# Kernel optimization log

Measured on AMD Instinct MI355X. Metric: run time of the kernel, lower is better.

## Reference

```python
import jax, jax.numpy as jnp
import numpy as np

INPUT_SIZE = 968
HIDDEN = 128
ESP = 1e-6


def _gru_scan(xp, w_hh, b_hh):
    # xp: [T, B, 3H] precomputed input projections; returns [T, B, H]
    B = xp.shape[1]
    h0 = jnp.zeros((B, HIDDEN), dtype=xp.dtype)

    def step(h, xp_t):
        gi_r, gi_z, gi_n = jnp.split(xp_t, 3, axis=-1)
        gh = h @ w_hh.T + b_hh
        gh_r, gh_z, gh_n = jnp.split(gh, 3, axis=-1)
        r = jax.nn.sigmoid(gi_r + gh_r)
        z = jax.nn.sigmoid(gi_z + gh_z)
        n = jnp.tanh(gi_n + r * gh_n)
        h_new = (1.0 - z) * n + z * h
        return h_new, h_new

    _, hs = jax.lax.scan(step, h0, xp)
    return hs


def _bigru_ln(x, w_ih_f, w_hh_f, b_ih_f, b_hh_f,
              w_ih_b, w_hh_b, b_ih_b, b_hh_b, ln_w, ln_b):
    # x: [B, T, D] (batch_first)
    # precompute input projections as one big GEMM per direction
    xp_f = jnp.einsum('btd,gd->btg', x, w_ih_f) + b_ih_f  # [B,T,3H]
    xp_b = jnp.einsum('btd,gd->btg', x, w_ih_b) + b_ih_b
    xp_f = jnp.swapaxes(xp_f, 0, 1)  # [T,B,3H]
    xp_b = jnp.swapaxes(xp_b, 0, 1)[::-1]  # reversed time for backward dir

    h_f = _gru_scan(xp_f, w_hh_f, b_hh_f)          # [T,B,H]
    h_b = _gru_scan(xp_b, w_hh_b, b_hh_b)[::-1]    # [T,B,H], un-reverse

    out = jnp.concatenate([h_f, h_b], axis=-1)     # [T,B,2H]
    out = jnp.swapaxes(out, 0, 1)                  # [B,T,2H]

    # LayerNormal: uses unbiased std (torch.std default, ddof=1), clamped
    mu = jnp.mean(out, axis=-1, keepdims=True)
    sigma = jnp.std(out, axis=-1, keepdims=True, ddof=1)
    sigma = jnp.maximum(sigma, ESP)
    return (out - mu) / sigma * ln_w + ln_b


def setup_inputs() -> dict:
    key = jax.random.key(0)
    ks = jax.random.split(key, 10)
    B, T = 64, 512
    s_ih = 1.0 / np.sqrt(HIDDEN)
    u = lambda k, shape: jax.random.uniform(k, shape, jnp.float32, -s_ih, s_ih)
    return {
        'x': jax.random.normal(ks[0], (B, T, INPUT_SIZE), jnp.float32),
        'w_ih_f': u(ks[1], (3 * HIDDEN, INPUT_SIZE)),
        'w_hh_f': u(ks[2], (3 * HIDDEN, HIDDEN)),
        'b_ih_f': u(ks[3], (3 * HIDDEN,)),
        'b_hh_f': u(ks[4], (3 * HIDDEN,)),
        'w_ih_b': u(ks[5], (3 * HIDDEN, INPUT_SIZE)),
        'w_hh_b': u(ks[6], (3 * HIDDEN, HIDDEN)),
        'b_ih_b': u(ks[7], (3 * HIDDEN,)),
        'b_hh_b': u(ks[8], (3 * HIDDEN,)),
        'ln_w': jnp.ones((2 * HIDDEN,), jnp.float32),
        'ln_b': jnp.zeros((2 * HIDDEN,), jnp.float32),
    }


def reference(x, w_ih_f, w_hh_f, b_ih_f, b_hh_f,
              w_ih_b, w_hh_b, b_ih_b, b_hh_b, ln_w, ln_b):
    return _bigru_ln(x, w_ih_f, w_hh_f, b_ih_f, b_hh_f,
                     w_ih_b, w_hh_b, b_ih_b, b_hh_b, ln_w, ln_b)
```

## Files before the change

kernel.cpp:

```cpp
#include <hip/hip_runtime.h>
#include <stdint.h>


#define LOG2E 1.4426950408889634f
#define TT 512
#define D_IN 968
#define KP 992
#define NOUT 768
#define HID 128

typedef __attribute__((ext_vector_type(8))) short short8;
typedef __attribute__((ext_vector_type(4))) float f32x4;
typedef __attribute__((ext_vector_type(4))) unsigned int u32x4;
typedef __attribute__((ext_vector_type(2))) unsigned int u32x2;

__device__ __forceinline__ unsigned short f2bf(float f) {
  unsigned u = __builtin_bit_cast(unsigned, f);
  u += 0x7FFFu + ((u >> 16) & 1u);
  return (unsigned short)(u >> 16);
}
__device__ __forceinline__ unsigned pack2bf(float a, float b) {
  return (unsigned)f2bf(a) | ((unsigned)f2bf(b) << 16);
}
__device__ __forceinline__ float exp2_(float x) { return __builtin_amdgcn_exp2f(x); }
__device__ __forceinline__ float rcp_(float x)  { return __builtin_amdgcn_rcpf(x); }

__device__ __forceinline__ void async_load16(const void* g, void* l) {
  __builtin_amdgcn_global_load_lds(
      (const __attribute__((address_space(1))) unsigned int*)g,
      (__attribute__((address_space(3))) unsigned int*)l, 16, 0, 0);
}

__device__ __forceinline__ void wg_barrier_lds() {
  asm volatile("s_waitcnt lgkmcnt(0)\n\ts_barrier" ::: "memory");
}

#define WIH_BYTES (NOUT * KP * 2)
#define WHH_BYTES (NOUT * HID * 2)
#define BIAS_BYTES 3072
#define BASE_OFF (WIH_BYTES + WHH_BYTES + BIAS_BYTES)
#define XBF_BYTES ((size_t)32768 * KP * 2)
#define XP_BYTES ((size_t)32768 * NOUT * 4)

__global__ __launch_bounds__(256) void kx_convert(const float* __restrict__ X,
                                                  unsigned short* __restrict__ Xb) {
  const long row = blockIdx.x;
  const int t = threadIdx.x;
  if (t < 242) {
    f32x4 v = *(const f32x4*)(X + row * D_IN + t * 4);
    u32x2 p = {pack2bf(v.x, v.y), pack2bf(v.z, v.w)};
    *(u32x2*)(Xb + row * KP + t * 4) = p;
  } else if (t < 248) {
    *(u32x2*)(Xb + row * KP + t * 4) = (u32x2){0, 0};
  }
}

__global__ __launch_bounds__(256) void k0_convert(
    const float* __restrict__ wihf, const float* __restrict__ whhf,
    const float* __restrict__ bihf, const float* __restrict__ wihb,
    const float* __restrict__ whhb, const float* __restrict__ bihb,
    unsigned short* __restrict__ wih16, unsigned short* __restrict__ whh16,
    float* __restrict__ bias_s) {
  int blk = blockIdx.x, tid = threadIdx.x;
  if (blk < NOUT) {
    int n = blk;
    float sc = ((n % 384) < 256) ? LOG2E : 2.0f * LOG2E;
    const float* src = (n < 384) ? (wihf + (long)n * D_IN) : (wihb + (long)(n - 384) * D_IN);
    for (int c = 0; c < 4; c++) {
      int k = c * 256 + tid;
      if (k < KP) {
        float v = (k < D_IN) ? src[k] * sc : 0.0f;
        wih16[(long)n * KP + k] = f2bf(v);
      }
    }
  } else if (blk < NOUT + 96) {
    int e0 = ((blk - NOUT) * 256 + tid) * 4;
    for (int i = 0; i < 4; i++) {
      int e = e0 + i;
      int m = e >> 7, k = e & 127;
      float sc = ((m % 384) < 256) ? LOG2E : 2.0f * LOG2E;
      float v = (m < 384) ? whhf[m * HID + k] : whhb[(m - 384) * HID + k];
      whh16[e] = f2bf(v * sc);
    }
  } else {
    for (int c = 0; c < 3; c++) {
      int n = c * 256 + tid;
      if (n < NOUT) {
        float sc = ((n % 384) < 256) ? LOG2E : 2.0f * LOG2E;
        bias_s[n] = ((n < 384) ? bihf[n] : bihb[n - 384]) * sc;
      }
    }
  }
}

__global__ __launch_bounds__(256, 2) void k1_gemm_fast(
    const unsigned short* __restrict__ Xb, const unsigned short* __restrict__ W,
    const float* __restrict__ bias_s, float* __restrict__ XP) {
  __shared__ unsigned short As[128 * 32];
  __shared__ unsigned short Bs[128 * 32];

  const int tid = threadIdx.x;
  const int lane = tid & 63, w = tid >> 6;
  const int q = lane >> 4, l15 = lane & 15;
  const int wr = w >> 1, wc = w & 1;
  const int nt = blockIdx.x;
  const int mt = blockIdx.y;
  const long R0 = (long)mt * 128;
  const int C0 = nt * 128;

  f32x4 acc[4][4];
#pragma unroll
  for (int i = 0; i < 4; i++)
#pragma unroll
    for (int j = 0; j < 4; j++) acc[i][j] = {0.f, 0.f, 0.f, 0.f};

  for (int it = 0; it < 31; it++) {
    const int k0 = it * 32;
#pragma unroll
    for (int c = 0; c < 2; c++) {
      int idx = c * 256 + w * 64 + lane;
      int row = idx >> 2, koff = (idx & 3) * 8;
      async_load16(Xb + (R0 + row) * KP + k0 + koff,
                   ((char*)As) + (c * 256 + w * 64) * 16);
      async_load16(W + (long)(C0 + row) * KP + k0 + koff,
                   ((char*)Bs) + (c * 256 + w * 64) * 16);
    }
    __syncthreads();
    short8 af[4], bf[4];
#pragma unroll
    for (int i = 0; i < 4; i++)
      af[i] = *(const short8*)&As[(wr * 64 + i * 16 + l15) * 32 + q * 8];
#pragma unroll
    for (int j = 0; j < 4; j++)
      bf[j] = *(const short8*)&Bs[(wc * 64 + j * 16 + l15) * 32 + q * 8];
#pragma unroll
    for (int i = 0; i < 4; i++)
#pragma unroll
      for (int j = 0; j < 4; j++)
        acc[i][j] = __builtin_amdgcn_mfma_f32_16x16x32_bf16(af[i], bf[j], acc[i][j], 0, 0, 0);
    __syncthreads();
  }
  float bv[4];
#pragma unroll
  for (int j = 0; j < 4; j++) bv[j] = bias_s[C0 + wc * 64 + j * 16 + l15];
#pragma unroll
  for (int i = 0; i < 4; i++)
#pragma unroll
    for (int j = 0; j < 4; j++) {
      int col = C0 + wc * 64 + j * 16 + l15;
      long Rb = R0 + wr * 64 + i * 16 + q * 4;
#pragma unroll
      for (int r = 0; r < 4; r++)
        XP[(Rb + r) * NOUT + col] = acc[i][j][r] + bv[j];
    }
}

#define AS_STRIDE 40
__global__ __launch_bounds__(256, 2) void k1_gemm_slow(
    const float* __restrict__ X, const unsigned short* __restrict__ W,
    const float* __restrict__ bias_s, float* __restrict__ XP) {
  __shared__ unsigned short As[128 * AS_STRIDE];
  __shared__ unsigned short Bs[128 * 32];
  const int tid = threadIdx.x;
  const int lane = tid & 63, w = tid >> 6;
  const int q = lane >> 4, l15 = lane & 15;
  const int wr = w >> 1, wc = w & 1;
  const int nt = blockIdx.x, mt = blockIdx.y;
  const long R0 = (long)mt * 128;
  const int C0 = nt * 128;
  const int ar = tid >> 1, ahf = tid & 1;
  f32x4 acc[4][4];
#pragma unroll
  for (int i = 0; i < 4; i++)
#pragma unroll
    for (int j = 0; j < 4; j++) acc[i][j] = {0.f, 0.f, 0.f, 0.f};
  const float* arow = X + (R0 + ar) * D_IN;
  for (int it = 0; it < 31; it++) {
    int k0 = it * 32;
    unsigned pk[8];
#pragma unroll
    for (int c = 0; c < 4; c++) {
      int kc = k0 + ahf * 16 + c * 4;
      kc = (kc <= 964) ? kc : 964;
      f32x4 v = *(const f32x4*)(arow + kc);
      pk[c * 2 + 0] = pack2bf(v.x, v.y);
      pk[c * 2 + 1] = pack2bf(v.z, v.w);
    }
    unsigned short* adst = &As[ar * AS_STRIDE + ahf * 16];
    *(u32x4*)adst = (u32x4){pk[0], pk[1], pk[2], pk[3]};
    *(u32x4*)(adst + 8) = (u32x4){pk[4], pk[5], pk[6], pk[7]};
#pragma unroll
    for (int c = 0; c < 2; c++) {
      int idx = c * 256 + w * 64 + lane;
      int brow = idx >> 2, koff = (idx & 3) * 8;
      async_load16(W + (long)(C0 + brow) * KP + k0 + koff,
                   ((char*)Bs) + (c * 256 + w * 64) * 16);
    }
    __syncthreads();
    short8 af[4], bf[4];
#pragma unroll
    for (int i = 0; i < 4; i++)
      af[i] = *(const short8*)&As[(wr * 64 + i * 16 + l15) * AS_STRIDE + q * 8];
#pragma unroll
    for (int j = 0; j < 4; j++)
      bf[j] = *(const short8*)&Bs[(wc * 64 + j * 16 + l15) * 32 + q * 8];
#pragma unroll
    for (int i = 0; i < 4; i++)
#pragma unroll
      for (int j = 0; j < 4; j++)
        acc[i][j] = __builtin_amdgcn_mfma_f32_16x16x32_bf16(af[i], bf[j], acc[i][j], 0, 0, 0);
    __syncthreads();
  }
  float bv[4];
#pragma unroll
  for (int j = 0; j < 4; j++) bv[j] = bias_s[C0 + wc * 64 + j * 16 + l15];
#pragma unroll
  for (int i = 0; i < 4; i++)
#pragma unroll
    for (int j = 0; j < 4; j++) {
      int col = C0 + wc * 64 + j * 16 + l15;
      long Rb = R0 + wr * 64 + i * 16 + q * 4;
#pragma unroll
      for (int r = 0; r < 4; r++)
        XP[(Rb + r) * NOUT + col] = acc[i][j][r] + bv[j];
    }
}

#define GI_STRIDE 52

__global__ __launch_bounds__(512) void k2_gru(
    const unsigned short* __restrict__ WHH, const float* __restrict__ XP,
    const float* __restrict__ bhh_f, const float* __restrict__ bhh_b,
    float* __restrict__ OUT) {
  __shared__ unsigned short Hl[2][16 * 128];
  __shared__ float GIl[2][8][16 * GI_STRIDE];

  const int tid = threadIdx.x;
  const int lane = tid & 63, w = tid >> 6;
  const int q = lane >> 4, b = lane & 15;
  const int dir = blockIdx.x & 1, bg = blockIdx.x >> 1;
  const int j0 = w * 16 + q * 4;

  for (int i = tid; i < 2 * 16 * 128; i += 512) ((unsigned short*)Hl)[i] = 0;

  short8 afr[3][4];
#pragma unroll
  for (int g = 0; g < 3; g++)
#pragma unroll
    for (int kt = 0; kt < 4; kt++) {
      int row = dir * 384 + g * 128 + w * 16 + b;
      afr[g][kt] = *(const short8*)(WHH + (long)row * HID + kt * 32 + q * 8);
    }
  const float* bhh = dir ? bhh_b : bhh_f;
  f32x4 bh[3];
#pragma unroll
  for (int g = 0; g < 3; g++) {
    f32x4 t = *(const f32x4*)(bhh + g * 128 + j0);
    bh[g] = t * ((g < 2) ? LOG2E : 2.0f * LOG2E);
  }

  const int lb = lane >> 2, lc = lane & 3;
  const long gi_base = (long)(bg * 16 + lb) * TT * NOUT + dir * 384 + w * 16 + lc * 4;
  const long out_base = (long)(bg * 16 + b) * TT * 256 + dir * 128 + j0;

  f32x4 gp0, gp1, gp2;
  {
    const int td0 = dir ? (TT - 1) : 0;
    const float* gb = XP + gi_base + (long)td0 * NOUT;
    f32x4 a0 = *(const f32x4*)(gb);
    f32x4 a1 = *(const f32x4*)(gb + 128);
    f32x4 a2 = *(const f32x4*)(gb + 256);
    float* giw0 = &GIl[0][w][lb * GI_STRIDE + lc * 4];
    *(f32x4*)(giw0 + 0) = a0;
    *(f32x4*)(giw0 + 16) = a1;
    *(f32x4*)(giw0 + 32) = a2;
    const int td1 = dir ? (TT - 2) : 1;
    const float* gb1 = XP + gi_base + (long)td1 * NOUT;
    gp0 = *(const f32x4*)(gb1);
    gp1 = *(const f32x4*)(gb1 + 128);
    gp2 = *(const f32x4*)(gb1 + 256);
  }
  f32x4 h = {0.f, 0.f, 0.f, 0.f};
  __syncthreads();

  for (int t = 0; t < TT; t++) {
    const int cur = t & 1, nxt = cur ^ 1;
    const int td = dir ? (TT - 1 - t) : t;

    short8 bfr[4];
#pragma unroll
    for (int kt = 0; kt < 4; kt++) {
      int ch = ((kt * 4 + q) ^ (b & 7)) * 8;
      bfr[kt] = *(const short8*)&Hl[cur][b * 128 + ch];
    }
    {
      float* giw = &GIl[nxt][w][lb * GI_STRIDE + lc * 4];
      *(f32x4*)(giw + 0) = gp0;
      *(f32x4*)(giw + 16) = gp1;
      *(f32x4*)(giw + 32) = gp2;
    }
    {
      int tn2 = (t + 2 < TT) ? t + 2 : TT - 1;
      int tdn2 = dir ? (TT - 1 - tn2) : tn2;
      const float* gb = XP + gi_base + (long)tdn2 * NOUT;
      gp0 = *(const f32x4*)(gb);
      gp1 = *(const f32x4*)(gb + 128);
      gp2 = *(const f32x4*)(gb + 256);
    }
    f32x4 accR = {0.f, 0.f, 0.f, 0.f};
    f32x4 accZ = {0.f, 0.f, 0.f, 0.f};
    f32x4 accN = {0.f, 0.f, 0.f, 0.f};
#pragma unroll
    for (int kt = 0; kt < 4; kt++) {
      accR = __builtin_amdgcn_mfma_f32_16x16x32_bf16(afr[0][kt], bfr[kt], accR, 0, 0, 0);
      accZ = __builtin_amdgcn_mfma_f32_16x16x32_bf16(afr[1][kt], bfr[kt], accZ, 0, 0, 0);
      accN = __builtin_amdgcn_mfma_f32_16x16x32_bf16(afr[2][kt], bfr[kt], accN, 0, 0, 0);
    }
    const float* gir = &GIl[cur][w][b * GI_STRIDE];
    f32x4 gr = *(const f32x4*)(gir + 0 + q * 4);
    f32x4 gz = *(const f32x4*)(gir + 16 + q * 4);
    f32x4 gn = *(const f32x4*)(gir + 32 + q * 4);
    f32x4 hnew;
#pragma unroll
    for (int i = 0; i < 4; i++) {
      float pr = gr[i] + accR[i] + bh[0][i];
      float pz = gz[i] + accZ[i] + bh[1][i];
      float r = rcp_(1.0f + exp2_(-pr));
      float z = rcp_(1.0f + exp2_(-pz));
      float pn = gn[i] + r * (accN[i] + bh[2][i]);
      float n = 1.0f - 2.0f * rcp_(exp2_(pn) + 1.0f);
      hnew[i] = n + z * (h[i] - n);
    }
    h = hnew;
    {
      int ch = ((j0 >> 3) ^ (b & 7)) * 8 + (j0 & 7);
      u32x2 hv = {pack2bf(hnew[0], hnew[1]), pack2bf(hnew[2], hnew[3])};
      *(u32x2*)&Hl[nxt][b * 128 + ch] = hv;
    }
    *(f32x4*)(OUT + out_base + (long)td * 256) = hnew;
    wg_barrier_lds();
  }
}

__global__ __launch_bounds__(256) void k3_ln(float* __restrict__ OUT,
                                             const float* __restrict__ lnw,
                                             const float* __restrict__ lnb) {
  const int tid = threadIdx.x, lane = tid & 63, w = tid >> 6;
  const long row = (long)blockIdx.x * 4 + w;
  float* p = OUT + row * 256 + lane * 4;
  f32x4 x = *(const f32x4*)p;
  float s = x[0] + x[1] + x[2] + x[3];
  float s2 = x[0] * x[0] + x[1] * x[1] + x[2] * x[2] + x[3] * x[3];
#pragma unroll
  for (int m = 1; m < 64; m <<= 1) {
    s += __shfl_xor(s, m, 64);
    s2 += __shfl_xor(s2, m, 64);
  }
  float mu = s * (1.0f / 256.0f);
  float var = (s2 - s * mu) * (1.0f / 255.0f);
  var = fmaxf(var, 0.0f);
  float sig = fmaxf(sqrtf(var), 1e-6f);
  float inv = 1.0f / sig;
  f32x4 wv = *(const f32x4*)(lnw + lane * 4);
  f32x4 bv = *(const f32x4*)(lnb + lane * 4);
  f32x4 y;
#pragma unroll
  for (int i = 0; i < 4; i++) y[i] = (x[i] - mu) * inv * wv[i] + bv[i];
  *(f32x4*)p = y;
}

extern "C" void kernel_launch(void* const* d_in, const int* in_sizes, int n_in,
                              void* d_out, int out_size, void* d_ws, size_t ws_size,
                              hipStream_t stream) {
  const float* x = (const float*)d_in[0];
  const float* wihf = (const float*)d_in[1];
  const float* whhf = (const float*)d_in[2];
  const float* bihf = (const float*)d_in[3];
  const float* bhhf = (const float*)d_in[4];
  const float* wihb = (const float*)d_in[5];
  const float* whhb = (const float*)d_in[6];
  const float* bihb = (const float*)d_in[7];
  const float* bhhb = (const float*)d_in[8];
  const float* lnw = (const float*)d_in[9];
  const float* lnb = (const float*)d_in[10];

  char* ws = (char*)d_ws;
  unsigned short* wih16 = (unsigned short*)ws;
  unsigned short* whh16 = (unsigned short*)(ws + WIH_BYTES);
  float* bias_s = (float*)(ws + WIH_BYTES + WHH_BYTES);
  float* out = (float*)d_out;

  const size_t need_fast = (size_t)BASE_OFF + XBF_BYTES + XP_BYTES;

  hipLaunchKernelGGL(k0_convert, dim3(768 + 96 + 1), dim3(256), 0, stream,
                     wihf, whhf, bihf, wihb, whhb, bihb, wih16, whh16, bias_s);

  float* xp;
  if (ws_size >= need_fast) {
    unsigned short* xbf = (unsigned short*)(ws + BASE_OFF);
    xp = (float*)(ws + BASE_OFF + XBF_BYTES);
    hipLaunchKernelGGL(kx_convert, dim3(32768), dim3(256), 0, stream, x, xbf);
    hipLaunchKernelGGL(k1_gemm_fast, dim3(6, 256), dim3(256), 0, stream,
                       xbf, wih16, bias_s, xp);
  } else {
    xp = (float*)(ws + BASE_OFF);
    hipLaunchKernelGGL(k1_gemm_slow, dim3(6, 256), dim3(256), 0, stream,
                       x, wih16, bias_s, xp);
  }
  hipLaunchKernelGGL(k2_gru, dim3(8), dim3(512), 0, stream, whh16, xp, bhhf, bhhb, out);
  hipLaunchKernelGGL(k3_ln, dim3(8192), dim3(256), 0, stream, out, lnw, lnb);
}
```

Baseline: 678.2 us.

## Load GRU input projections directly into MFMA layout registers, drop LDS staging

The GRU recurrence kernel no longer stages the precomputed input projections through an LDS buffer. Each lane now loads its own gate values from global memory straight into the MFMA accumulator layout, with a two-step register double-buffer and the loop unrolled by two. The input and hidden biases are folded into the MFMA initial accumulators. The sigmoid pair shares one reciprocal via the product of denominators, and the barrier asm no longer carries a memory clobber. This removes LDS writes, reads and pressure from the serial per-step critical path, in exchange for more register use and a less conservative barrier.

```diff
diff --git a/kernel.cpp b/kernel.cpp
--- a/kernel.cpp
+++ b/kernel.cpp
@@ -11,6 +11,7 @@
 
 typedef __attribute__((ext_vector_type(8))) short short8;
 typedef __attribute__((ext_vector_type(4))) float f32x4;
+typedef __attribute__((ext_vector_type(2))) float f32x2;
 typedef __attribute__((ext_vector_type(4))) unsigned int u32x4;
 typedef __attribute__((ext_vector_type(2))) unsigned int u32x2;
 
@@ -31,8 +32,8 @@
       (__attribute__((address_space(3))) unsigned int*)l, 16, 0, 0);
 }
 
-__device__ __forceinline__ void wg_barrier_lds() {
-  asm volatile("s_waitcnt lgkmcnt(0)\n\ts_barrier" ::: "memory");
+__device__ __forceinline__ void bar_lds() {
+  asm volatile("s_waitcnt lgkmcnt(0)\n\ts_barrier");
 }
 
 #define WIH_BYTES (NOUT * KP * 2)
@@ -226,14 +227,11 @@
     }
 }
 
-#define GI_STRIDE 52
-
 __global__ __launch_bounds__(512) void k2_gru(
     const unsigned short* __restrict__ WHH, const float* __restrict__ XP,
     const float* __restrict__ bhh_f, const float* __restrict__ bhh_b,
     float* __restrict__ OUT) {
   __shared__ unsigned short Hl[2][16 * 128];
-  __shared__ float GIl[2][8][16 * GI_STRIDE];
 
   const int tid = threadIdx.x;
   const int lane = tid & 63, w = tid >> 6;
@@ -259,86 +257,88 @@
     bh[g] = t * ((g < 2) ? LOG2E : 2.0f * LOG2E);
   }
 
-  const int lb = lane >> 2, lc = lane & 3;
-  const long gi_base = (long)(bg * 16 + lb) * TT * NOUT + dir * 384 + w * 16 + lc * 4;
+  const float* gi_ptr = XP + (long)(bg * 16 + b) * TT * NOUT + dir * 384 + w * 16 + q * 4;
   const long out_base = (long)(bg * 16 + b) * TT * 256 + dir * 128 + j0;
 
-  f32x4 gp0, gp1, gp2;
+  f32x4 gp[2][3];
   {
     const int td0 = dir ? (TT - 1) : 0;
-    const float* gb = XP + gi_base + (long)td0 * NOUT;
-    f32x4 a0 = *(const f32x4*)(gb);
-    f32x4 a1 = *(const f32x4*)(gb + 128);
-    f32x4 a2 = *(const f32x4*)(gb + 256);
-    float* giw0 = &GIl[0][w][lb * GI_STRIDE + lc * 4];
-    *(f32x4*)(giw0 + 0) = a0;
-    *(f32x4*)(giw0 + 16) = a1;
-    *(f32x4*)(giw0 + 32) = a2;
     const int td1 = dir ? (TT - 2) : 1;
-    const float* gb1 = XP + gi_base + (long)td1 * NOUT;
-    gp0 = *(const f32x4*)(gb1);
-    gp1 = *(const f32x4*)(gb1 + 128);
-    gp2 = *(const f32x4*)(gb1 + 256);
+    const float* p0 = gi_ptr + (long)td0 * NOUT;
+    const float* p1 = gi_ptr + (long)td1 * NOUT;
+#pragma unroll
+    for (int g = 0; g < 3; g++) gp[0][g] = *(const f32x4*)(p0 + g * 128);
+#pragma unroll
+    for (int g = 0; g < 3; g++) gp[1][g] = *(const f32x4*)(p1 + g * 128);
   }
   f32x4 h = {0.f, 0.f, 0.f, 0.f};
   __syncthreads();
 
-  for (int t = 0; t < TT; t++) {
-    const int cur = t & 1, nxt = cur ^ 1;
-    const int td = dir ? (TT - 1 - t) : t;
-
-    short8 bfr[4];
-#pragma unroll
-    for (int kt = 0; kt < 4; kt++) {
-      int ch = ((kt * 4 + q) ^ (b & 7)) * 8;
-      bfr[kt] = *(const short8*)&Hl[cur][b * 128 + ch];
-    }
-    {
-      float* giw = &GIl[nxt][w][lb * GI_STRIDE + lc * 4];
-      *(f32x4*)(giw + 0) = gp0;
-      *(f32x4*)(giw + 16) = gp1;
-      *(f32x4*)(giw + 32) = gp2;
-    }
-    {
-      int tn2 = (t + 2 < TT) ? t + 2 : TT - 1;
-      int tdn2 = dir ? (TT - 1 - tn2) : tn2;
-      const float* gb = XP + gi_base + (long)tdn2 * NOUT;
-      gp0 = *(const f32x4*)(gb);
-      gp1 = *(const f32x4*)(gb + 128);
-      gp2 = *(const f32x4*)(gb + 256);
-    }
-    f32x4 accR = {0.f, 0.f, 0.f, 0.f};
-    f32x4 accZ = {0.f, 0.f, 0.f, 0.f};
-    f32x4 accN = {0.f, 0.f, 0.f, 0.f};
-#pragma unroll
-    for (int kt = 0; kt < 4; kt++) {
-      accR = __builtin_amdgcn_mfma_f32_16x16x32_bf16(afr[0][kt], bfr[kt], accR, 0, 0, 0);
-      accZ = __builtin_amdgcn_mfma_f32_16x16x32_bf16(afr[1][kt], bfr[kt], accZ, 0, 0, 0);
-      accN = __builtin_amdgcn_mfma_f32_16x16x32_bf16(afr[2][kt], bfr[kt], accN, 0, 0, 0);
-    }
-    const float* gir = &GIl[cur][w][b * GI_STRIDE];
-    f32x4 gr = *(const f32x4*)(gir + 0 + q * 4);
-    f32x4 gz = *(const f32x4*)(gir + 16 + q * 4);
-    f32x4 gn = *(const f32x4*)(gir + 32 + q * 4);
-    f32x4 hnew;
-#pragma unroll
-    for (int i = 0; i < 4; i++) {
-      float pr = gr[i] + accR[i] + bh[0][i];
-      float pz = gz[i] + accZ[i] + bh[1][i];
-      float r = rcp_(1.0f + exp2_(-pr));
-      float z = rcp_(1.0f + exp2_(-pz));
-      float pn = gn[i] + r * (accN[i] + bh[2][i]);
-      float n = 1.0f - 2.0f * rcp_(exp2_(pn) + 1.0f);
-      hnew[i] = n + z * (h[i] - n);
-    }
-    h = hnew;
-    {
-      int ch = ((j0 >> 3) ^ (b & 7)) * 8 + (j0 & 7);
-      u32x2 hv = {pack2bf(hnew[0], hnew[1]), pack2bf(hnew[2], hnew[3])};
-      *(u32x2*)&Hl[nxt][b * 128 + ch] = hv;
-    }
-    *(f32x4*)(OUT + out_base + (long)td * 256) = hnew;
-    wg_barrier_lds();
+  for (int tb = 0; tb < TT; tb += 2) {
+#pragma unroll
+    for (int u = 0; u < 2; u++) {
+      const int t = tb + u;
+      const int cur = u, nxt = u ^ 1;
+      const int td = dir ? (TT - 1 - t) : t;
+
+      short8 bfr[4];
+#pragma unroll
+      for (int kt = 0; kt < 4; kt++) {
+        int ch = ((kt * 4 + q) ^ (b & 7)) * 8;
+        bfr[kt] = *(const short8*)&Hl[cur][b * 128 + ch];
+      }
+      f32x4 accR = gp[u][0] + bh[0];
+      f32x4 accZ = gp[u][1] + bh[1];
+      f32x4 gn = gp[u][2];
+      f32x4 accN = bh[2];
+      {
+        const int t2 = (t + 2 < TT) ? t + 2 : TT - 1;
+        const int td2 = dir ? (TT - 1 - t2) : t2;
+        const float* p2 = gi_ptr + (long)td2 * NOUT;
+        gp[u][0] = *(const f32x4*)(p2);
+        gp[u][1] = *(const f32x4*)(p2 + 128);
+        gp[u][2] = *(const f32x4*)(p2 + 256);
+      }
+#pragma unroll
+      for (int kt = 0; kt < 4; kt++) {
+        accR = __builtin_amdgcn_mfma_f32_16x16x32_bf16(afr[0][kt], bfr[kt], accR, 0, 0, 0);
+        accZ = __builtin_amdgcn_mfma_f32_16x16x32_bf16(afr[1][kt], bfr[kt], accZ, 0, 0, 0);
+        accN = __builtin_amdgcn_mfma_f32_16x16x32_bf16(afr[2][kt], bfr[kt], accN, 0, 0, 0);
+      }
+      f32x4 hnew;
+#pragma unroll
+      for (int p = 0; p < 2; p++) {
+        f32x2 pr = {accR[2 * p], accR[2 * p + 1]};
+        f32x2 pz = {accZ[2 * p], accZ[2 * p + 1]};
+        f32x2 an = {accN[2 * p], accN[2 * p + 1]};
+        f32x2 gn2 = {gn[2 * p], gn[2 * p + 1]};
+        f32x2 h2 = {h[2 * p], h[2 * p + 1]};
+        f32x2 ea = {exp2_(-pr.x), exp2_(-pr.y)};
+        f32x2 eb = {exp2_(-pz.x), exp2_(-pz.y)};
+        f32x2 A = ea + 1.0f;
+        f32x2 B = eb + 1.0f;
+        f32x2 P = A * B;
+        f32x2 ip = {rcp_(P.x), rcp_(P.y)};
+        f32x2 r = ip * B;
+        f32x2 z = ip * A;
+        f32x2 pn = gn2 + r * an;
+        f32x2 E = {exp2_(pn.x), exp2_(pn.y)};
+        f32x2 Dn = E + 1.0f;
+        f32x2 iD = {rcp_(Dn.x), rcp_(Dn.y)};
+        f32x2 n = 1.0f - 2.0f * iD;
+        f32x2 hn = n + z * (h2 - n);
+        hnew[2 * p] = hn.x;
+        hnew[2 * p + 1] = hn.y;
+      }
+      h = hnew;
+      {
+        int ch = ((j0 >> 3) ^ (b & 7)) * 8 + (j0 & 7);
+        u32x2 hv = {pack2bf(hnew[0], hnew[1]), pack2bf(hnew[2], hnew[3])};
+        *(u32x2*)&Hl[nxt][b * 128 + ch] = hv;
+      }
+      *(f32x4*)(OUT + out_base + (long)td * 256) = hnew;
+      bar_lds();
+    }
   }
 }
 
```

After: 764.1 us. 1.13x slower.
